# Kernel tuning notes

Measured on AMD Instinct MI355X. Metric: run time of the kernel, lower is better.

Reference implementation:

```python
import jax, jax.numpy as jnp
import numpy as np
import math

NUM_HEADS = 8
KEY_DIM = 32
VALUE_DIM = 32
ERF = 3                      # local window (erf x erf), N = 1 + ERF*ERF key/query positions
PAD = (ERF - 1) // 2
STRIDE = 2
OUT_CH = 256


def unfold_2d(x, k, p, s):
    """Mirror of F.unfold -> (B, k*k, C, Ho, Wo), window index row-major (kh, kw)."""
    B, C, H, W = x.shape
    xp = jnp.pad(x, ((0, 0), (0, 0), (p, p), (p, p)))
    Ho = (H + 2 * p - k) // s + 1
    Wo = (W + 2 * p - k) // s + 1
    pats = [xp[:, :, i:i + s * (Ho - 1) + 1:s, j:j + s * (Wo - 1) + 1:s]
            for i in range(k) for j in range(k)]
    return jnp.stack(pats, axis=1)


def fold_2d(pats, out_hw, k, p, s):
    """Mirror of F.fold (overlap-add inverse of unfold_2d)."""
    B, kk, C, Ho, Wo = pats.shape
    H, W = out_hw
    out = jnp.zeros((B, C, H + 2 * p, W + 2 * p), pats.dtype)
    idx = 0
    for i in range(k):
        for j in range(k):
            out = out.at[:, :, i:i + s * (Ho - 1) + 1:s, j:j + s * (Wo - 1) + 1:s].add(pats[:, idx])
            idx += 1
    return out[:, :, p:p + H, p:p + W]


def setup_inputs() -> dict:
    key = jax.random.key(0)
    ks = jax.random.split(key, 10)
    B = 2
    d = {
        "top_feat": jax.random.normal(ks[0], (B, OUT_CH, 64, 64), jnp.float32),
        "bot_feat": jax.random.normal(ks[1], (B, OUT_CH, 128, 128), jnp.float32),
    }
    qkv_names = ["W_top_key", "W_top_query", "W_top_value", "W_bot_key", "W_bot_query", "W_bot_value"]
    for n, kk in zip(qkv_names, ks[2:8]):
        out_dim = NUM_HEADS * (KEY_DIM if ("key" in n or "query" in n) else VALUE_DIM)
        d[n] = 0.01 * jax.random.normal(kk, (out_dim, OUT_CH), jnp.float32)  # 1x1 conv, no bias
    d["W_top_fuse"] = 0.01 * jax.random.normal(ks[8], (OUT_CH, NUM_HEADS * VALUE_DIM), jnp.float32)
    d["W_bot_fuse"] = 0.01 * jax.random.normal(ks[9], (OUT_CH, NUM_HEADS * VALUE_DIM), jnp.float32)
    return d


def _forward(top_feat, bot_feat, W_top_key, W_top_query, W_top_value,
             W_bot_key, W_bot_query, W_bot_value, W_top_fuse, W_bot_fuse):
    B, _, H, W = top_feat.shape
    Hb, Wb = bot_feat.shape[2], bot_feat.shape[3]

    def proj(x, Wm, dim):  # 1x1 conv then split heads -> (B, h, dim, H', W')
        y = jnp.einsum('oc,bchw->bohw', Wm, x)
        return y.reshape(B, NUM_HEADS, dim, x.shape[2], x.shape[3])

    def unfold_heads(x):  # (B, h, d, Hb, Wb) -> (B, h, e*e, d, H, W)
        d = x.shape[2]
        u = unfold_2d(x.reshape(B * NUM_HEADS, d, Hb, Wb), ERF, PAD, STRIDE)
        return u.reshape(B, NUM_HEADS, ERF * ERF, d, u.shape[3], u.shape[4])

    tK = proj(top_feat, W_top_key, KEY_DIM)[:, :, None]      # (B, h, 1, kd, H, W)
    tQ = proj(top_feat, W_top_query, KEY_DIM)[:, :, None]
    tV = proj(top_feat, W_top_value, VALUE_DIM)[:, :, None]
    bK = unfold_heads(proj(bot_feat, W_bot_key, KEY_DIM))    # (B, h, e*e, kd, H, W)
    bQ = unfold_heads(proj(bot_feat, W_bot_query, KEY_DIM))
    bV = unfold_heads(proj(bot_feat, W_bot_value, VALUE_DIM))

    key_ = jnp.concatenate([tK, bK], axis=2)   # (B, h, N, kd, H, W), N = 1 + e*e
    query = jnp.concatenate([tQ, bQ], axis=2)
    value = jnp.concatenate([tV, bV], axis=2)

    # weight[b,n,k,q,h,w] = <key_k, query_q> / sqrt(kd)   (NOTE: no softmax in original)
    weight = jnp.einsum('bnkdhw,bnqdhw->bnkqhw', key_, query) / math.sqrt(KEY_DIM)
    # out[b,n,q,v,h,w] = sum_k weight[...] * value_k
    out = jnp.einsum('bnkqhw,bnkvhw->bnqvhw', weight, value)  # (B, h, N, vd, H, W)

    top_ret = out[:, :, 0].reshape(B, NUM_HEADS * VALUE_DIM, H, W)
    bot_pat = out[:, :, 1:].reshape(B * NUM_HEADS, ERF * ERF, VALUE_DIM, H, W)
    bot_ret = fold_2d(bot_pat, (Hb, Wb), ERF, PAD, STRIDE).reshape(B, NUM_HEADS * VALUE_DIM, Hb, Wb)

    top_out = jnp.einsum('oc,bchw->bohw', W_top_fuse, top_ret)
    bot_out = jnp.einsum('oc,bchw->bohw', W_bot_fuse, bot_ret)
    return top_out, bot_out


def reference(top_feat, bot_feat, W_top_key, W_top_query, W_top_value,
              W_bot_key, W_bot_query, W_bot_value, W_top_fuse, W_bot_fuse):
    return _forward(top_feat, bot_feat, W_top_key, W_top_query, W_top_value,
                    W_bot_key, W_bot_query, W_bot_value, W_top_fuse, W_bot_fuse)
```

## Files before the change

### kernel.cpp

```cpp
#include <hip/hip_runtime.h>
#include <hip/hip_bf16.h>
#include <math.h>


typedef __attribute__((ext_vector_type(8))) short  bh8;
typedef __attribute__((ext_vector_type(4))) short  bh4;
typedef __attribute__((ext_vector_type(4))) float  f32x4;
typedef unsigned short u16;

static __device__ __forceinline__ u16 f2b(float x) {
    __hip_bfloat16 h = __float2bfloat16(x);
    return __builtin_bit_cast(u16, h);
}
static __device__ __forceinline__ float b2f(u16 u) {
    unsigned v = ((unsigned)u) << 16;
    return __builtin_bit_cast(float, v);
}

static __device__ __forceinline__ void gload16(const u16* g, u16* l) {
    __builtin_amdgcn_global_load_lds(
        (const __attribute__((address_space(1))) unsigned int*)g,
        (__attribute__((address_space(3))) unsigned int*)l, 16, 0, 0);
}

__global__ __launch_bounds__(256) void k_cvt_w(
    const float* w0, const float* w1, const float* w2, const float* w3,
    const float* w4, const float* w5, const float* w6, const float* w7,
    u16* __restrict__ Wb)
{
    const float* srcs[8] = {w0,w1,w2,w3,w4,w5,w6,w7};
    const float* src = srcs[blockIdx.y];
    int i = (blockIdx.x * 256 + threadIdx.x) * 4;
    float4 v = *(const float4*)&src[i];
    u16 tmp[4] = { f2b(v.x), f2b(v.y), f2b(v.z), f2b(v.w) };
    *(uint2*)&Wb[(size_t)blockIdx.y * 65536 + i] = *(uint2*)tmp;
}

__global__ __launch_bounds__(256) void k_proj(
    const float* __restrict__ top_feat, const float* __restrict__ bot_feat,
    const u16* __restrict__ Wb,
    u16* __restrict__ tK, u16* __restrict__ bK, size_t TOPU, size_t BOTU)
{
    const int yb    = blockIdx.y;
    const bool istop = yb < 128;
    const float* feat = istop ? top_feat : bot_feat;
    const u16* Bw   = istop ? Wb : (Wb + 3 * 65536);
    u16* Yp         = istop ? tK : bK;
    const size_t arrsz = istop ? TOPU : BOTU;
    const int S     = istop ? 4096 : 16384;
    const int m0g   = (istop ? yb : (yb - 128)) * 64;
    const int b     = istop ? (m0g >> 12) : (m0g >> 14);
    const int pix0  = m0g & (S - 1);
    const float* Xb = feat + (size_t)b * 256 * S;
    const int n0 = blockIdx.x * 256;
    const int t  = threadIdx.x;
    const int w  = t >> 6, wl = t & 63, l16 = wl & 15, grp = wl >> 4;
    const int apix = t & 63;
    const int aq   = t >> 6;

    __shared__ __align__(16) u16 AT[2][64 * 32];

    float rA[8];

#define PA_LOAD(kk) do {                                                      \
        _Pragma("unroll")                                                     \
        for (int e = 0; e < 8; ++e)                                           \
            rA[e] = Xb[(size_t)((kk) + aq * 8 + e) * S + pix0 + apix];        \
    } while (0)

#define PA_WRITE(bufi) do {                                                   \
        u16 tmp[8];                                                           \
        _Pragma("unroll")                                                     \
        for (int e = 0; e < 8; ++e) tmp[e] = f2b(rA[e]);                      \
        int slot = aq ^ ((apix >> 1) & 3);                                    \
        *(uint4*)&AT[bufi][apix * 32 + slot * 8] = *(uint4*)tmp;              \
    } while (0)

    f32x4 acc[4][4];
    #pragma unroll
    for (int i = 0; i < 4; ++i)
        #pragma unroll
        for (int j = 0; j < 4; ++j) acc[i][j] = (f32x4){0.f, 0.f, 0.f, 0.f};

    const u16* BwRow = Bw + (size_t)(n0 + w * 64 + l16) * 256;

    PA_LOAD(0);
    PA_WRITE(0);
    int cur = 0;
    for (int kt = 0; kt < 8; ++kt) {
        __syncthreads();
        if (kt < 7) PA_LOAD((kt + 1) * 32);

        bh8 bf[4];
        #pragma unroll
        for (int ni = 0; ni < 4; ++ni)
            bf[ni] = *(const bh8*)(BwRow + (size_t)ni * 16 * 256
                                   + kt * 32 + grp * 8);
        bh8 af[4];
        #pragma unroll
        for (int mi = 0; mi < 4; ++mi) {
            int row = mi * 16 + l16;
            int slot = grp ^ ((row >> 1) & 3);
            af[mi] = *(const bh8*)&AT[cur][row * 32 + slot * 8];
        }
        #pragma unroll
        for (int mi = 0; mi < 4; ++mi)
            #pragma unroll
            for (int ni = 0; ni < 4; ++ni)
                acc[mi][ni] = __builtin_amdgcn_mfma_f32_16x16x32_bf16(
                    af[mi], bf[ni], acc[mi][ni], 0, 0, 0);
        if (kt < 7) PA_WRITE(cur ^ 1);
        cur ^= 1;
    }
#undef PA_LOAD
#undef PA_WRITE

    #pragma unroll
    for (int mi = 0; mi < 4; ++mi)
        #pragma unroll
        for (int ni = 0; ni < 4; ++ni)
            #pragma unroll
            for (int r = 0; r < 4; ++r) {
                int m = m0g + mi*16 + grp*4 + r;
                int n = n0 + w*64 + ni*16 + l16;
                Yp[(size_t)(n >> 8) * arrsz + (size_t)m * 256 + (n & 255)]
                    = f2b(acc[mi][ni][r]);
            }
}

#define GEMM_STAGE(bufi, kk) do {                                             \
        _Pragma("unroll")                                                     \
        for (int it = 0; it < 2; ++it) {                                      \
            int lin = it * 256 + t;                                           \
            int row = lin >> 3, c = lin & 7;                                  \
            int cs = c ^ (row & 7);                                           \
            gload16(&A[(size_t)(m0 + row) * 256 + (kk) + cs * 8],             \
                    &AT[bufi][lin * 8]);                                      \
        }                                                                     \
        _Pragma("unroll")                                                     \
        for (int it = 0; it < 8; ++it) {                                      \
            int lin = it * 256 + t;                                           \
            int row = lin >> 3, c = lin & 7;                                  \
            int cs = c ^ (row & 7);                                           \
            gload16(&B[(size_t)(n0 + row) * 256 + (kk) + cs * 8],             \
                    &BT[bufi][lin * 8]);                                      \
        }                                                                     \
    } while (0)

#define GEMM_MAIN()                                                           \
    GEMM_STAGE(0, 0);                                                         \
    int cur = 0;                                                              \
    for (int kt = 0; kt < 4; ++kt) {                                          \
        __syncthreads();                                                      \
        if (kt < 3) GEMM_STAGE(cur ^ 1, (kt + 1) * 64);                       \
        _Pragma("unroll")                                                     \
        for (int ks = 0; ks < 2; ++ks) {                                      \
            bh8 af[4], bf[4];                                                 \
            _Pragma("unroll")                                                 \
            for (int mi = 0; mi < 4; ++mi) {                                  \
                int row = mi * 16 + l16;                                      \
                int pc = (ks * 4 + grp) ^ (row & 7);                          \
                af[mi] = *(const bh8*)&AT[cur][row * 64 + pc * 8];            \
            }                                                                 \
            _Pragma("unroll")                                                 \
            for (int ni = 0; ni < 4; ++ni) {                                  \
                int row = w * 64 + ni * 16 + l16;                             \
                int pc = (ks * 4 + grp) ^ (row & 7);                          \
                bf[ni] = *(const bh8*)&BT[cur][row * 64 + pc * 8];            \
            }                                                                 \
            _Pragma("unroll")                                                 \
            for (int mi = 0; mi < 4; ++mi)                                    \
                _Pragma("unroll")                                             \
                for (int ni = 0; ni < 4; ++ni)                                \
                    acc[mi][ni] = __builtin_amdgcn_mfma_f32_16x16x32_bf16(    \
                        af[mi], bf[ni], acc[mi][ni], 0, 0, 0);                \
        }                                                                     \
        cur ^= 1;                                                             \
    }

__global__ __launch_bounds__(256) void k_fuse(
    const u16* __restrict__ Wb, const u16* __restrict__ tRet,
    const u16* __restrict__ botRet, float* __restrict__ top_out,
    float* __restrict__ bot_out)
{
    const int bid = blockIdx.x;
    const u16* A; const u16* B; float* Yf; int lgS, n0, m0;
    if (bid < 128) {
        A = Wb + 6 * 65536; B = tRet; Yf = top_out; lgS = 12;
        n0 = (bid & 31) * 256; m0 = (bid >> 5) * 64;
    } else {
        int i = bid - 128;
        A = Wb + 7 * 65536; B = botRet; Yf = bot_out; lgS = 14;
        n0 = (i & 127) * 256; m0 = (i >> 7) * 64;
    }
    const int t  = threadIdx.x;
    const int w  = t >> 6, wl = t & 63, l16 = wl & 15, grp = wl >> 4;

    __shared__ __align__(16) u16 AT[2][64 * 64];
    __shared__ __align__(16) u16 BT[2][256 * 64];

    f32x4 acc[4][4];
    #pragma unroll
    for (int i = 0; i < 4; ++i)
        #pragma unroll
        for (int j = 0; j < 4; ++j) acc[i][j] = (f32x4){0.f, 0.f, 0.f, 0.f};

    GEMM_MAIN();

    #pragma unroll
    for (int mi = 0; mi < 4; ++mi)
        #pragma unroll
        for (int ni = 0; ni < 4; ++ni)
            #pragma unroll
            for (int r = 0; r < 4; ++r) {
                int m = m0 + mi*16 + grp*4 + r;
                int n = n0 + w*64 + ni*16 + l16;
                int bb = n >> lgS, s = n & ((1 << lgS) - 1);
                Yf[(((size_t)bb * 256 + m) << lgS) + s] = acc[mi][ni][r];
            }
}

__global__ __launch_bounds__(256) void k_attn(
    const u16* __restrict__ tK, const u16* __restrict__ tQ, const u16* __restrict__ tV,
    const u16* __restrict__ bK, const u16* __restrict__ bQ, const u16* __restrict__ bV,
    u16* __restrict__ tRet, u16* __restrict__ pat)
{
    const int pix = blockIdx.x;
    const int b   = blockIdx.y;
    const int w   = threadIdx.x >> 6;
    const int wl  = threadIdx.x & 63;
    const int l16 = wl & 15, grp = wl >> 4;
    const int y = pix >> 6, x = pix & 63;

    __shared__ u16 Ssm[4][16][24];
    __shared__ __align__(16) u16 Vsm[4][2][16][16];

    const int p = l16;
    bool pvalid = false; int bpix = 0; const bool istop = (p == 0);
    if (p == 0) pvalid = true;
    else if (p < 10) {
        int pm = p - 1; int i = (pm * 11) >> 5; int j = pm - 3 * i;
        int by = 2 * y + i - 1, bx = 2 * x + j - 1;
        pvalid = ((unsigned)by < 128u) && ((unsigned)bx < 128u);
        bpix = by * 128 + bx;
    }
    const size_t topRow = ((size_t)b * 4096  + pix)  * 256;
    const size_t botRow = ((size_t)b * 16384 + bpix) * 256;
    const float scale = 0.17677669529663687f;

    #pragma unroll
    for (int hi = 0; hi < 2; ++hi) {
        const int h = w + hi * 4;
        const size_t off = (istop ? topRow : botRow) + h * 32 + grp * 8;
        bh8 aQ = {}, aK = {}, vV = {};
        if (pvalid) {
            if (istop) {
                aQ = *(const bh8*)(tQ + off);
                aK = *(const bh8*)(tK + off);
                vV = *(const bh8*)(tV + off);
            } else {
                aQ = *(const bh8*)(bQ + off);
                aK = *(const bh8*)(bK + off);
                vV = *(const bh8*)(bV + off);
            }
        }
        *(bh8*)&Vsm[w][grp >> 1][p][(grp & 1) * 8] = vV;

        f32x4 z = {0.f, 0.f, 0.f, 0.f};
        f32x4 sC = __builtin_amdgcn_mfma_f32_16x16x32_bf16(aQ, aK, z, 0, 0, 0);
        #pragma unroll
        for (int r = 0; r < 4; ++r)
            Ssm[w][grp * 4 + r][l16] = f2b(sC[r] * scale);

        bh8 aS = {};
        *(bh4*)&aS = *(const bh4*)&Ssm[w][l16][grp * 4];

        bh8 bv0 = {}, bv1 = {};
        #pragma unroll
        for (int j = 0; j < 4; ++j) {
            bv0[j] = (short)Vsm[w][0][grp * 4 + j][l16];
            bv1[j] = (short)Vsm[w][1][grp * 4 + j][l16];
        }
        f32x4 oc0 = __builtin_amdgcn_mfma_f32_16x16x32_bf16(aS, bv0, z, 0, 0, 0);
        f32x4 oc1 = __builtin_amdgcn_mfma_f32_16x16x32_bf16(aS, bv1, z, 0, 0, 0);

        if (grp == 0) {
            size_t o = topRow + (size_t)h * 32;
            tRet[o + l16]      = f2b(oc0[0]);
            tRet[o + 16 + l16] = f2b(oc1[0]);
        }
        #pragma unroll
        for (int r = 0; r < 4; ++r) {
            int q = grp * 4 + r;
            if (q >= 1 && q <= 9) {
                size_t base = ((((size_t)b * 8 + h) * 9 + (q - 1)) * 4096 + pix) * 32;
                pat[base + l16]      = f2b(oc0[r]);
                pat[base + 16 + l16] = f2b(oc1[r]);
            }
        }
    }
}

__global__ __launch_bounds__(256) void k_fold(
    const u16* __restrict__ pat, u16* __restrict__ botRet)
{
    int tid = blockIdx.x * 256 + threadIdx.x;
    int vchunk = tid & 3;
    int ri = tid >> 2;
    int b = ri >> 17;
    int bpix = (ri >> 3) & 16383;
    int h = ri & 7;
    int by = bpix >> 7, bx = bpix & 127;
    int v0 = vchunk * 8;

    float acc[8];
    #pragma unroll
    for (int e = 0; e < 8; ++e) acc[e] = 0.f;

    for (int iy = 0; iy < 3; ++iy) {
        int ty = by + 1 - iy;
        if (ty & 1) continue;
        int yy = ty >> 1;
        if ((unsigned)yy >= 64u) continue;
        for (int jx = 0; jx < 3; ++jx) {
            int tx = bx + 1 - jx;
            if (tx & 1) continue;
            int xx = tx >> 1;
            if ((unsigned)xx >= 64u) continue;
            int q = iy * 3 + jx;
            size_t addr = ((((size_t)b * 8 + h) * 9 + q) * 4096 + (yy * 64 + xx)) * 32 + v0;
            uint4 pv = *(const uint4*)&pat[addr];
            const u16* pp = (const u16*)&pv;
            #pragma unroll
            for (int e = 0; e < 8; ++e) acc[e] += b2f(pp[e]);
        }
    }
    u16 tmp[8];
    #pragma unroll
    for (int e = 0; e < 8; ++e) tmp[e] = f2b(acc[e]);
    *(uint4*)&botRet[((size_t)b * 16384 + bpix) * 256 + h * 32 + v0] = *(uint4*)tmp;
}

extern "C" void kernel_launch(void* const* d_in, const int* in_sizes, int n_in,
                              void* d_out, int out_size, void* d_ws, size_t ws_size,
                              hipStream_t stream) {
    const float* top_feat = (const float*)d_in[0];
    const float* bot_feat = (const float*)d_in[1];

    float* out     = (float*)d_out;
    float* top_out = out;
    float* bot_out = out + (size_t)2 * 256 * 4096;

    const size_t TOPU = (size_t)2 * 4096  * 256;
    const size_t BOTU = (size_t)2 * 16384 * 256;
    char* p = (char*)d_ws;
    u16* Wb     = (u16*)p;  p += (size_t)8 * 65536 * 2;
    u16* tK     = (u16*)p;  p += TOPU * 2;
    u16* tQ     = (u16*)p;  p += TOPU * 2;
    u16* tV     = (u16*)p;  p += TOPU * 2;
    u16* bK     = (u16*)p;  p += BOTU * 2;
    u16* bQ     = (u16*)p;  p += BOTU * 2;
    u16* bV     = (u16*)p;  p += BOTU * 2;
    u16* tRet   = (u16*)p;  p += TOPU * 2;
    u16* pat    = (u16*)p;  p += (size_t)2*8*9*4096*32*2;
    u16* botRet = (u16*)p;  p += BOTU * 2;

    dim3 blk(256);

    k_cvt_w<<<dim3(64, 8), blk, 0, stream>>>(
        (const float*)d_in[2], (const float*)d_in[3], (const float*)d_in[4],
        (const float*)d_in[5], (const float*)d_in[6], (const float*)d_in[7],
        (const float*)d_in[8], (const float*)d_in[9], Wb);

    k_proj<<<dim3(3, 640), blk, 0, stream>>>(top_feat, bot_feat, Wb,
                                             tK, bK, TOPU, BOTU);

    k_attn<<<dim3(4096, 2), blk, 0, stream>>>(tK, tQ, tV, bK, bQ, bV, tRet, pat);

    k_fold<<<dim3(4096), blk, 0, stream>>>(pat, botRet);

    k_fuse<<<dim3(640), blk, 0, stream>>>(Wb, tRet, botRet, top_out, bot_out);
}
```

Before: 109.9 us.

## Remap block IDs across XCDs and load projection A-tiles directly from global

Blocks of the projection, attention and fold kernels are remapped so that consecutive logical blocks land on the same XCD (block id mod 8 chooses a contiguous chunk). This aims to improve L2 locality on the multi-die GPU. The projection kernel also drops its LDS double-buffered A tile and the barrier, and instead has each lane read eight strided fp32 values straight from global memory per MFMA fragment. That removes LDS traffic and synchronisation, but adds redundant global loads because each warp now reads the A tile itself, and the loads are less coalesced.

```diff
diff --git a/kernel.cpp b/kernel.cpp
--- a/kernel.cpp
+++ b/kernel.cpp
@@ -41,7 +41,9 @@
     const u16* __restrict__ Wb,
     u16* __restrict__ tK, u16* __restrict__ bK, size_t TOPU, size_t BOTU)
 {
-    const int yb    = blockIdx.y;
+    const int lbid  = (blockIdx.x & 7) * 240 + (blockIdx.x >> 3);
+    const int yb    = lbid / 3;
+    const int n0    = (lbid - yb * 3) * 256;
     const bool istop = yb < 128;
     const float* feat = istop ? top_feat : bot_feat;
     const u16* Bw   = istop ? Wb : (Wb + 3 * 65536);
@@ -51,30 +53,11 @@
     const int m0g   = (istop ? yb : (yb - 128)) * 64;
     const int b     = istop ? (m0g >> 12) : (m0g >> 14);
     const int pix0  = m0g & (S - 1);
-    const float* Xb = feat + (size_t)b * 256 * S;
-    const int n0 = blockIdx.x * 256;
     const int t  = threadIdx.x;
     const int w  = t >> 6, wl = t & 63, l16 = wl & 15, grp = wl >> 4;
-    const int apix = t & 63;
-    const int aq   = t >> 6;
-
-    __shared__ __align__(16) u16 AT[2][64 * 32];
-
-    float rA[8];
-
-#define PA_LOAD(kk) do {                                                      \
-        _Pragma("unroll")                                                     \
-        for (int e = 0; e < 8; ++e)                                           \
-            rA[e] = Xb[(size_t)((kk) + aq * 8 + e) * S + pix0 + apix];        \
-    } while (0)
-
-#define PA_WRITE(bufi) do {                                                   \
-        u16 tmp[8];                                                           \
-        _Pragma("unroll")                                                     \
-        for (int e = 0; e < 8; ++e) tmp[e] = f2b(rA[e]);                      \
-        int slot = aq ^ ((apix >> 1) & 3);                                    \
-        *(uint4*)&AT[bufi][apix * 32 + slot * 8] = *(uint4*)tmp;              \
-    } while (0)
+
+    const float* Xl = feat + (size_t)b * 256 * S + pix0 + l16;
+    const u16*   Bl = Bw + (size_t)(n0 + w * 64 + l16) * 256 + grp * 8;
 
     f32x4 acc[4][4];
     #pragma unroll
@@ -82,26 +65,20 @@
         #pragma unroll
         for (int j = 0; j < 4; ++j) acc[i][j] = (f32x4){0.f, 0.f, 0.f, 0.f};
 
-    const u16* BwRow = Bw + (size_t)(n0 + w * 64 + l16) * 256;
-
-    PA_LOAD(0);
-    PA_WRITE(0);
-    int cur = 0;
     for (int kt = 0; kt < 8; ++kt) {
-        __syncthreads();
-        if (kt < 7) PA_LOAD((kt + 1) * 32);
-
+        const size_t kc = (size_t)(kt * 32 + grp * 8) * S;
         bh8 bf[4];
         #pragma unroll
         for (int ni = 0; ni < 4; ++ni)
-            bf[ni] = *(const bh8*)(BwRow + (size_t)ni * 16 * 256
-                                   + kt * 32 + grp * 8);
+            bf[ni] = *(const bh8*)(Bl + (size_t)ni * 16 * 256 + kt * 32);
         bh8 af[4];
         #pragma unroll
         for (int mi = 0; mi < 4; ++mi) {
-            int row = mi * 16 + l16;
-            int slot = grp ^ ((row >> 1) & 3);
-            af[mi] = *(const bh8*)&AT[cur][row * 32 + slot * 8];
+            bh8 a;
+            #pragma unroll
+            for (int e = 0; e < 8; ++e)
+                a[e] = (short)f2b(Xl[kc + (size_t)e * S + mi * 16]);
+            af[mi] = a;
         }
         #pragma unroll
         for (int mi = 0; mi < 4; ++mi)
@@ -109,11 +86,7 @@
             for (int ni = 0; ni < 4; ++ni)
                 acc[mi][ni] = __builtin_amdgcn_mfma_f32_16x16x32_bf16(
                     af[mi], bf[ni], acc[mi][ni], 0, 0, 0);
-        if (kt < 7) PA_WRITE(cur ^ 1);
-        cur ^= 1;
-    }
-#undef PA_LOAD
-#undef PA_WRITE
+    }
 
     #pragma unroll
     for (int mi = 0; mi < 4; ++mi)
@@ -225,8 +198,9 @@
     const u16* __restrict__ bK, const u16* __restrict__ bQ, const u16* __restrict__ bV,
     u16* __restrict__ tRet, u16* __restrict__ pat)
 {
-    const int pix = blockIdx.x;
-    const int b   = blockIdx.y;
+    const int lbid = (blockIdx.x & 7) * 1024 + (blockIdx.x >> 3);
+    const int pix = lbid & 4095;
+    const int b   = lbid >> 12;
     const int w   = threadIdx.x >> 6;
     const int wl  = threadIdx.x & 63;
     const int l16 = wl & 15, grp = wl >> 4;
@@ -304,7 +278,8 @@
 __global__ __launch_bounds__(256) void k_fold(
     const u16* __restrict__ pat, u16* __restrict__ botRet)
 {
-    int tid = blockIdx.x * 256 + threadIdx.x;
+    const int lbid = (blockIdx.x & 7) * 512 + (blockIdx.x >> 3);
+    int tid = lbid * 256 + threadIdx.x;
     int vchunk = tid & 3;
     int ri = tid >> 2;
     int b = ri >> 17;
@@ -365,19 +340,17 @@
     u16* pat    = (u16*)p;  p += (size_t)2*8*9*4096*32*2;
     u16* botRet = (u16*)p;  p += BOTU * 2;
 
-    dim3 blk(256);
-
-    k_cvt_w<<<dim3(64, 8), blk, 0, stream>>>(
+    k_cvt_w<<<dim3(64, 8), dim3(256), 0, stream>>>(
         (const float*)d_in[2], (const float*)d_in[3], (const float*)d_in[4],
         (const float*)d_in[5], (const float*)d_in[6], (const float*)d_in[7],
         (const float*)d_in[8], (const float*)d_in[9], Wb);
 
-    k_proj<<<dim3(3, 640), blk, 0, stream>>>(top_feat, bot_feat, Wb,
-                                             tK, bK, TOPU, BOTU);
-
-    k_attn<<<dim3(4096, 2), blk, 0, stream>>>(tK, tQ, tV, bK, bQ, bV, tRet, pat);
-
-    k_fold<<<dim3(4096), blk, 0, stream>>>(pat, botRet);
-
-    k_fuse<<<dim3(640), blk, 0, stream>>>(Wb, tRet, botRet, top_out, bot_out);
-}
+    k_proj<<<dim3(1920), dim3(256), 0, stream>>>(top_feat, bot_feat, Wb,
+                                                 tK, bK, TOPU, BOTU);
+
+    k_attn<<<dim3(8192), dim3(256), 0, stream>>>(tK, tQ, tV, bK, bQ, bV, tRet, pat);
+
+    k_fold<<<dim3(4096), dim3(256), 0, stream>>>(pat, botRet);
+
+    k_fuse<<<dim3(640), dim3(256), 0, stream>>>(Wb, tRet, botRet, top_out, bot_out);
+}
```

Measured after the change: 111.1 us. No clear change (+1.1%).
